# Optimization experiments

Hardware: AMD Instinct MI355X
Metric: run time of the kernel (lower is better)

Reference implementation:

```python
import jax, jax.numpy as jnp
import numpy as np

EPS = 1e-6

def act_quant(x):
    # per-token int8 absmax quantization with straight-through estimator
    scale = 127.0 / jnp.clip(jnp.max(jnp.abs(x), axis=-1, keepdims=True), 1e-5)
    q = jnp.clip(jnp.round(x * scale), -128.0, 127.0) / scale
    return x + jax.lax.stop_gradient(q - x)

def weight_quant(w):
    # ternary absmean quantization with straight-through estimator
    scale = 1.0 / jnp.clip(jnp.mean(jnp.abs(w)), 1e-5)
    q = jnp.clip(jnp.round(w * scale), -1.0, 1.0) / scale
    return w + jax.lax.stop_gradient(q - w)

def bit_linear(x, w):
    # x: [..., in], w: [out, in]
    return jnp.einsum('...i,oi->...o', act_quant(x), weight_quant(w))

def subln(x, g):
    # RMSNorm over last dim with learnable gain
    var = jnp.mean(jnp.square(x), axis=-1, keepdims=True)
    return x * jax.lax.rsqrt(var + EPS) * g

def setup_inputs() -> dict:
    key = jax.random.key(0)
    k1, k2, k3 = jax.random.split(key, 3)
    B, S, H, I = 8, 8192, 512, 2048
    x = jax.random.normal(k1, (B, S, H), dtype=jnp.float32)
    w_up = jax.random.normal(k2, (I, H), dtype=jnp.float32) * (H ** -0.5)
    w_down = jax.random.normal(k3, (H, I), dtype=jnp.float32) * (I ** -0.5)
    g = jnp.ones((I,), dtype=jnp.float32)
    return {'x': x, 'w_up': w_up, 'w_down': w_down, 'g': g}

def reference(x, w_up, w_down, g):
    h = bit_linear(x, w_up)            # [B,S,I]
    h = jnp.square(jax.nn.relu(h))     # relu^2 activation
    h = subln(h, g)                    # SubLN (RMSNorm)
    return bit_linear(h, w_down)       # [B,S,H]
```

## Files before the change

### kernel.cpp

```cpp
#include <hip/hip_runtime.h>
#include <stdint.h>


typedef int v4i __attribute__((ext_vector_type(4)));

#define AS1(p) ((const __attribute__((address_space(1))) void*)(p))
#define AS3(p) ((__attribute__((address_space(3))) void*)(p))

static constexpr size_t OFF_PART = 256;
static constexpr size_t OFF_SX   = 8192;
static constexpr size_t OFF_RSQ  = OFF_SX   + 262144;
static constexpr size_t OFF_S2   = OFF_RSQ  + 262144;
static constexpr size_t OFF_INV2 = OFF_S2   + 262144;
static constexpr size_t OFF_WUQ  = OFF_INV2 + 262144;
static constexpr size_t OFF_WDQ  = OFF_WUQ  + 1048576;
static constexpr size_t OFF_XQ   = OFF_WDQ  + 1048576;
static constexpr size_t OFF_HQ   = OFF_XQ   + 33554432;
static constexpr size_t OFF_SS   = OFF_HQ   + 134217728;
static constexpr size_t OFF_MM   = OFF_SS   + 8388608;

__global__ void wabs_partial(const float* __restrict__ w, double* __restrict__ part)
{
    int t = threadIdx.x, bid = blockIdx.x;
    const float4* w4 = (const float4*)w;
    int base = bid * 256 + t;
    double s = 0.0;
    #pragma unroll
    for (int j = 0; j < 4; ++j) {
        float4 v = w4[base + j * 65536];
        s += (double)fabsf(v.x) + (double)fabsf(v.y)
           + (double)fabsf(v.z) + (double)fabsf(v.w);
    }
    #pragma unroll
    for (int off = 32; off > 0; off >>= 1) s += __shfl_down(s, off);
    __shared__ double ps[4];
    int l = t & 63, wv = t >> 6;
    if (l == 0) ps[wv] = s;
    __syncthreads();
    if (t == 0) part[bid] = ((ps[0] + ps[1]) + ps[2]) + ps[3];
}

__global__ void finalize_sums(const double* __restrict__ part, double* __restrict__ sums)
{
    int t = threadIdx.x;
    double a = part[t];
    double b = part[256 + t];
    #pragma unroll
    for (int off = 32; off > 0; off >>= 1) {
        a += __shfl_down(a, off);
        b += __shfl_down(b, off);
    }
    __shared__ double pa[4], pb[4];
    int l = t & 63, wv = t >> 6;
    if (l == 0) { pa[wv] = a; pb[wv] = b; }
    __syncthreads();
    if (t == 0) {
        sums[0] = ((pa[0] + pa[1]) + pa[2]) + pa[3];
        sums[1] = ((pb[0] + pb[1]) + pb[2]) + pb[3];
    }
}

__global__ void wquant(const float* __restrict__ w, const double* __restrict__ sum,
                       signed char* __restrict__ wq)
{
    int i = blockIdx.x * blockDim.x + threadIdx.x;
    if (i >= 262144) return;
    float mean  = (float)(*sum) * (1.0f / 1048576.0f);
    float scale = 1.0f / fmaxf(mean, 1e-5f);
    float4 v = ((const float4*)w)[i];
    int q0 = (int)fminf(fmaxf(rintf(v.x * scale), -1.f), 1.f);
    int q1 = (int)fminf(fmaxf(rintf(v.y * scale), -1.f), 1.f);
    int q2 = (int)fminf(fmaxf(rintf(v.z * scale), -1.f), 1.f);
    int q3 = (int)fminf(fmaxf(rintf(v.w * scale), -1.f), 1.f);
    unsigned pk = (q0 & 255) | ((q1 & 255) << 8) | ((q2 & 255) << 16) | ((q3 & 255) << 24);
    ((unsigned*)wq)[i] = pk;
}

__global__ void xquant(const float* __restrict__ x, signed char* __restrict__ xq,
                       float* __restrict__ inv_sx)
{
    int row = blockIdx.x * 4 + (threadIdx.x >> 6);
    int l   = threadIdx.x & 63;
    const float* xr = x + (size_t)row * 512;
    float4 v0 = *(const float4*)(xr + l * 8);
    float4 v1 = *(const float4*)(xr + l * 8 + 4);
    float m = fmaxf(fmaxf(fmaxf(fabsf(v0.x), fabsf(v0.y)), fmaxf(fabsf(v0.z), fabsf(v0.w))),
                    fmaxf(fmaxf(fabsf(v1.x), fabsf(v1.y)), fmaxf(fabsf(v1.z), fabsf(v1.w))));
    #pragma unroll
    for (int off = 1; off < 64; off <<= 1) m = fmaxf(m, __shfl_xor(m, off));
    float mc = fmaxf(m, 1e-5f);
    float s  = 127.0f / mc;
    int q[8];
    q[0] = (int)fminf(fmaxf(rintf(v0.x * s), -128.f), 127.f);
    q[1] = (int)fminf(fmaxf(rintf(v0.y * s), -128.f), 127.f);
    q[2] = (int)fminf(fmaxf(rintf(v0.z * s), -128.f), 127.f);
    q[3] = (int)fminf(fmaxf(rintf(v0.w * s), -128.f), 127.f);
    q[4] = (int)fminf(fmaxf(rintf(v1.x * s), -128.f), 127.f);
    q[5] = (int)fminf(fmaxf(rintf(v1.y * s), -128.f), 127.f);
    q[6] = (int)fminf(fmaxf(rintf(v1.z * s), -128.f), 127.f);
    q[7] = (int)fminf(fmaxf(rintf(v1.w * s), -128.f), 127.f);
    uint2 pk;
    pk.x = (q[0] & 255) | ((q[1] & 255) << 8) | ((q[2] & 255) << 16) | ((q[3] & 255) << 24);
    pk.y = (q[4] & 255) | ((q[5] & 255) << 8) | ((q[6] & 255) << 16) | ((q[7] & 255) << 24);
    *(uint2*)(xq + (size_t)row * 512 + l * 8) = pk;
    if (l == 0) inv_sx[row] = mc * (1.0f / 127.0f);
}

__global__ void row_reduce(const float* __restrict__ ss_p, const float* __restrict__ mm_p,
                           float* __restrict__ rsq, float* __restrict__ s2,
                           float* __restrict__ inv2)
{
    int row = blockIdx.x * blockDim.x + threadIdx.x;
    float ss = 0.f, mm = 0.f;
    #pragma unroll
    for (int p = 0; p < 32; ++p) {
        ss += ss_p[(size_t)row * 32 + p];
        mm  = fmaxf(mm, mm_p[(size_t)row * 32 + p]);
    }
    float var  = ss * (1.0f / 2048.0f);
    float r    = 1.0f / sqrtf(var + 1e-6f);
    float maxy = fmaxf(r * mm, 1e-5f);
    rsq[row]  = r;
    s2[row]   = 127.0f / maxy;
    inv2[row] = maxy * (1.0f / 127.0f);
}


#define PHASE(MH, NH, STAGE_STMT, TAIL_STMT)                                   \
  {                                                                            \
    v4i af[8]; v4i bf[4];                                                      \
    _Pragma("unroll")                                                          \
    for (int mm = 0; mm < 4; ++mm) {                                           \
      _Pragma("unroll")                                                        \
      for (int ks = 0; ks < 2; ++ks) {                                         \
        int r  = wr * 128 + ((MH) * 4 + mm) * 16 + lr;                         \
        int eg = (ks * 4 + lg) ^ lx;                                           \
        af[mm * 2 + ks] = *(const v4i*)(Ab + r * 128 + eg * 16);               \
      }                                                                        \
    }                                                                          \
    _Pragma("unroll")                                                          \
    for (int nn = 0; nn < 2; ++nn) {                                           \
      _Pragma("unroll")                                                        \
      for (int ks = 0; ks < 2; ++ks) {                                         \
        int r  = wc * 64 + ((NH) * 2 + nn) * 16 + lr;                          \
        int eg = (ks * 4 + lg) ^ lx;                                           \
        bf[nn * 2 + ks] = *(const v4i*)(Bb + r * 128 + eg * 16);               \
      }                                                                        \
    }                                                                          \
    STAGE_STMT;                                                                \
    __builtin_amdgcn_s_barrier();                                              \
    asm volatile("s_waitcnt lgkmcnt(0)" ::: "memory");                         \
    __builtin_amdgcn_sched_barrier(0);                                         \
    __builtin_amdgcn_s_setprio(1);                                             \
    _Pragma("unroll")                                                          \
    for (int mm = 0; mm < 4; ++mm)                                             \
      _Pragma("unroll")                                                        \
      for (int nn = 0; nn < 2; ++nn)                                           \
        _Pragma("unroll")                                                      \
        for (int ks = 0; ks < 2; ++ks)                                         \
          acc[(MH) * 4 + mm][(NH) * 2 + nn] =                                  \
              __builtin_amdgcn_mfma_i32_16x16x64_i8(                           \
                  af[mm * 2 + ks], bf[nn * 2 + ks],                            \
                  acc[(MH) * 4 + mm][(NH) * 2 + nn], 0, 0, 0);                 \
    __builtin_amdgcn_s_setprio(0);                                             \
    TAIL_STMT;                                                                 \
    __builtin_amdgcn_s_barrier();                                              \
  }

#define KTILE(KT, P)                                                           \
  {                                                                            \
    const char* Ab = &lds[P][0][0];                                            \
    const char* Bb = &lds[P][1][0];                                            \
    const int kt_ = (KT);                                                      \
    PHASE(0, 0, { if (kt_ + 1 < NKT) stageA((P) ^ 1, 1, kt_ + 1); }, {})       \
    PHASE(0, 1, { if (kt_ + 1 < NKT) stageB((P) ^ 1, 1, kt_ + 1); }, {})       \
    PHASE(1, 0, { if (kt_ + 2 < NKT) stageA((P), 0, kt_ + 2); }, {})           \
    PHASE(1, 1, { if (kt_ + 2 < NKT) stageB((P), 0, kt_ + 2); },               \
          {                                                                    \
            if (kt_ < NKT - 1) {                                               \
              if (kt_ + 2 < NKT)                                               \
                asm volatile("s_waitcnt vmcnt(4)" ::: "memory");               \
              else                                                             \
                asm volatile("s_waitcnt vmcnt(0)" ::: "memory");               \
            }                                                                  \
          })                                                                   \
  }

template<int K, int N, int EPI>
__global__ __launch_bounds__(512, 2)
void gemm_i8(const signed char* __restrict__ A,
             const signed char* __restrict__ B,
             const float* __restrict__ rowscale,
             const double* __restrict__ wsum,
             const float* __restrict__ g,
             const float* __restrict__ rsq,
             const float* __restrict__ s2,
             float* __restrict__ st_ss,
             float* __restrict__ st_mm,
             signed char* __restrict__ hq,
             float* __restrict__ out)
{
    constexpr int NKT = K / 128;
    constexpr int NBN = N / 256;
    __shared__ __align__(16) char lds[2][2][32768];

    int nwg  = gridDim.x;
    int orig = blockIdx.x;
    int q8 = nwg >> 3, r8 = nwg & 7;
    int xcd = orig & 7, lin = orig >> 3;
    int swz = (xcd < r8 ? xcd * (q8 + 1) : r8 * (q8 + 1) + (xcd - r8) * q8) + lin;
    int mt = swz / NBN, nt = swz - mt * NBN;

    size_t mbase = (size_t)mt * 256;
    int    nbase = nt * 256;

    int t  = threadIdx.x;
    int l  = t & 63;
    int wid = t >> 6;
    int wr = wid >> 2, wc = wid & 3;
    int lr = l & 15, lg = l >> 4, lx = l & 7;

    const signed char* Ag = A + mbase * K;
    const signed char* Bg = B + (size_t)nbase * K;

    auto stageA = [&](int buf, int sel, int ktt) {
        char* d0 = &lds[buf][0][0];
        #pragma unroll
        for (int i = 0; i < 2; ++i) {
            int j = i * 512 + t;
            int rho = j >> 3, gg = j & 7;
            int r = rho + (rho & 64) + sel * 64;
            int kg = gg ^ (r & 7);
            __builtin_amdgcn_global_load_lds(AS1(Ag + (size_t)r * K + ktt * 128 + kg * 16),
                                             AS3(d0 + r * 128 + gg * 16), 16, 0, 0);
        }
    };
    auto stageB = [&](int buf, int sel, int ktt) {
        char* d0 = &lds[buf][1][0];
        #pragma unroll
        for (int i = 0; i < 2; ++i) {
            int j = i * 512 + t;
            int rho = j >> 3, gg = j & 7;
            int r = ((rho & ~31) << 1) + (rho & 31) + sel * 32;
            int kg = gg ^ (r & 7);
            __builtin_amdgcn_global_load_lds(AS1(Bg + (size_t)r * K + ktt * 128 + kg * 16),
                                             AS3(d0 + r * 128 + gg * 16), 16, 0, 0);
        }
    };

    v4i acc[8][4] = {};

    stageA(0, 0, 0); stageB(0, 0, 0); stageA(0, 1, 0); stageB(0, 1, 0);
    if (NKT > 1) {
        stageA(1, 0, 1); stageB(1, 0, 1);
        asm volatile("s_waitcnt vmcnt(4)" ::: "memory");
    } else {
        asm volatile("s_waitcnt vmcnt(0)" ::: "memory");
    }
    __builtin_amdgcn_s_barrier();

    #pragma unroll 1
    for (int kt2 = 0; kt2 < NKT / 2; ++kt2) {
        int kt = kt2 * 2;
        KTILE(kt, 0)
        KTILE(kt + 1, 1)
    }

    float wmean = fmaxf((float)wsum[0] * (1.0f / 1048576.0f), 1e-5f);
    size_t rowb = mbase + (size_t)wr * 128;
    int    colb = nbase + wc * 64;

    if constexpr (EPI == 2) {
        #pragma unroll
        for (int m = 0; m < 8; ++m)
            #pragma unroll
            for (int reg = 0; reg < 4; ++reg) {
                size_t grow = rowb + m * 16 + lg * 4 + reg;
                float f = rowscale[grow] * wmean;
                #pragma unroll
                for (int n = 0; n < 4; ++n)
                    out[grow * N + colb + n * 16 + lr] = (float)acc[m][n][reg] * f;
            }
    } else {
        float gv[4];
        #pragma unroll
        for (int n = 0; n < 4; ++n) gv[n] = g[colb + n * 16 + lr];

        if constexpr (EPI == 0) {
            #pragma unroll
            for (int m = 0; m < 8; ++m)
                #pragma unroll
                for (int reg = 0; reg < 4; ++reg) {
                    size_t grow = rowb + m * 16 + lg * 4 + reg;
                    float f = rowscale[grow] * wmean;
                    float ss = 0.f, mx = 0.f;
                    #pragma unroll
                    for (int n = 0; n < 4; ++n) {
                        float z = (float)acc[m][n][reg] * f;
                        float a = fmaxf(z, 0.f);
                        float h = a * a;
                        ss += h * h;
                        mx  = fmaxf(mx, fabsf(h * gv[n]));
                    }
                    #pragma unroll
                    for (int off = 1; off < 16; off <<= 1) {
                        ss += __shfl_xor(ss, off);
                        mx  = fmaxf(mx, __shfl_xor(mx, off));
                    }
                    if (lr == 0) {
                        st_ss[grow * 32 + nt * 4 + wc] = ss;
                        st_mm[grow * 32 + nt * 4 + wc] = mx;
                    }
                }
        } else {
            #pragma unroll
            for (int m = 0; m < 8; ++m)
                #pragma unroll
                for (int reg = 0; reg < 4; ++reg) {
                    size_t grow = rowb + m * 16 + lg * 4 + reg;
                    float f  = rowscale[grow] * wmean;
                    float rq = rsq[grow];
                    float sc = s2[grow];
                    #pragma unroll
                    for (int n = 0; n < 4; ++n) {
                        float z = (float)acc[m][n][reg] * f;
                        float a = fmaxf(z, 0.f);
                        float h = a * a;
                        float y = (h * rq) * gv[n];
                        int qv = (int)fminf(fmaxf(rintf(y * sc), -128.f), 127.f);
                        hq[grow * 2048 + colb + n * 16 + lr] = (signed char)qv;
                    }
                }
        }
    }
}

extern "C" void kernel_launch(void* const* d_in, const int* in_sizes, int n_in,
                              void* d_out, int out_size, void* d_ws, size_t ws_size,
                              hipStream_t stream)
{
    const float* x  = (const float*)d_in[0];
    const float* wu = (const float*)d_in[1];
    const float* wd = (const float*)d_in[2];
    const float* g  = (const float*)d_in[3];
    float* out = (float*)d_out;
    char*  ws  = (char*)d_ws;

    double* sums     = (double*)ws;
    double* part     = (double*)(ws + OFF_PART);
    float*  inv_sx   = (float*)(ws + OFF_SX);
    float*  rsq      = (float*)(ws + OFF_RSQ);
    float*  s2       = (float*)(ws + OFF_S2);
    float*  inv2     = (float*)(ws + OFF_INV2);
    signed char* wuq = (signed char*)(ws + OFF_WUQ);
    signed char* wdq = (signed char*)(ws + OFF_WDQ);
    signed char* xq  = (signed char*)(ws + OFF_XQ);
    signed char* hq  = (signed char*)(ws + OFF_HQ);
    float*  st_ss    = (float*)(ws + OFF_SS);
    float*  st_mm    = (float*)(ws + OFF_MM);

    wabs_partial<<<256, 256, 0, stream>>>(wu, part);
    wabs_partial<<<256, 256, 0, stream>>>(wd, part + 256);
    finalize_sums<<<1, 256, 0, stream>>>(part, sums);
    wquant<<<1024, 256, 0, stream>>>(wu, sums + 0, wuq);
    wquant<<<1024, 256, 0, stream>>>(wd, sums + 1, wdq);
    xquant<<<16384, 256, 0, stream>>>(x, xq, inv_sx);

    gemm_i8<512, 2048, 0><<<2048, 512, 0, stream>>>(xq, wuq, inv_sx, sums + 0, g,
                                                    nullptr, nullptr, st_ss, st_mm,
                                                    nullptr, nullptr);
    row_reduce<<<256, 256, 0, stream>>>(st_ss, st_mm, rsq, s2, inv2);
    gemm_i8<512, 2048, 1><<<2048, 512, 0, stream>>>(xq, wuq, inv_sx, sums + 0, g,
                                                    rsq, s2, nullptr, nullptr,
                                                    hq, nullptr);
    gemm_i8<2048, 512, 2><<<512, 512, 0, stream>>>(hq, wdq, inv2, sums + 1,
                                                   nullptr, nullptr, nullptr,
                                                   nullptr, nullptr, nullptr, out);
}
```

Measured before the change: 597.2 us.

## Switch int8 GEMM to 32x32x32 MFMA with K=64 tiles and simpler pipeline

Replaces the 16x16x64 int8 MFMA tiling with 32x32x32 MFMA instructions, halving the K-tile to 64 bytes and shrinking LDS from 128KB to 64KB. The hand-tuned four-phase pipeline with split A/B staging, setprio and fine-grained vmcnt waits is replaced by a simple double buffer with __syncthreads between stages. Epilogue index mapping and the row reduction shuffle width change to match the 32x32 accumulator layout. The aim is fewer LDS fragment reads per MFMA and lower LDS footprint, at the cost of losing the finer overlap of loads and compute.

```diff
diff --git a/kernel.cpp b/kernel.cpp
--- a/kernel.cpp
+++ b/kernel.cpp
@@ -2,7 +2,8 @@
 #include <stdint.h>
 
 
-typedef int v4i __attribute__((ext_vector_type(4)));
+typedef int v4i  __attribute__((ext_vector_type(4)));
+typedef int v16i __attribute__((ext_vector_type(16)));
 
 #define AS1(p) ((const __attribute__((address_space(1))) void*)(p))
 #define AS3(p) ((__attribute__((address_space(3))) void*)(p))
@@ -126,64 +127,32 @@
 }
 
 
-#define PHASE(MH, NH, STAGE_STMT, TAIL_STMT)                                   \
-  {                                                                            \
-    v4i af[8]; v4i bf[4];                                                      \
-    _Pragma("unroll")                                                          \
-    for (int mm = 0; mm < 4; ++mm) {                                           \
-      _Pragma("unroll")                                                        \
-      for (int ks = 0; ks < 2; ++ks) {                                         \
-        int r  = wr * 128 + ((MH) * 4 + mm) * 16 + lr;                         \
-        int eg = (ks * 4 + lg) ^ lx;                                           \
-        af[mm * 2 + ks] = *(const v4i*)(Ab + r * 128 + eg * 16);               \
-      }                                                                        \
-    }                                                                          \
-    _Pragma("unroll")                                                          \
-    for (int nn = 0; nn < 2; ++nn) {                                           \
-      _Pragma("unroll")                                                        \
-      for (int ks = 0; ks < 2; ++ks) {                                         \
-        int r  = wc * 64 + ((NH) * 2 + nn) * 16 + lr;                          \
-        int eg = (ks * 4 + lg) ^ lx;                                           \
-        bf[nn * 2 + ks] = *(const v4i*)(Bb + r * 128 + eg * 16);               \
-      }                                                                        \
-    }                                                                          \
-    STAGE_STMT;                                                                \
-    __builtin_amdgcn_s_barrier();                                              \
-    asm volatile("s_waitcnt lgkmcnt(0)" ::: "memory");                         \
-    __builtin_amdgcn_sched_barrier(0);                                         \
-    __builtin_amdgcn_s_setprio(1);                                             \
-    _Pragma("unroll")                                                          \
-    for (int mm = 0; mm < 4; ++mm)                                             \
-      _Pragma("unroll")                                                        \
-      for (int nn = 0; nn < 2; ++nn)                                           \
-        _Pragma("unroll")                                                      \
-        for (int ks = 0; ks < 2; ++ks)                                         \
-          acc[(MH) * 4 + mm][(NH) * 2 + nn] =                                  \
-              __builtin_amdgcn_mfma_i32_16x16x64_i8(                           \
-                  af[mm * 2 + ks], bf[nn * 2 + ks],                            \
-                  acc[(MH) * 4 + mm][(NH) * 2 + nn], 0, 0, 0);                 \
-    __builtin_amdgcn_s_setprio(0);                                             \
-    TAIL_STMT;                                                                 \
-    __builtin_amdgcn_s_barrier();                                              \
-  }
-
-#define KTILE(KT, P)                                                           \
+#define COMPUTE(P)                                                             \
   {                                                                            \
     const char* Ab = &lds[P][0][0];                                            \
     const char* Bb = &lds[P][1][0];                                            \
-    const int kt_ = (KT);                                                      \
-    PHASE(0, 0, { if (kt_ + 1 < NKT) stageA((P) ^ 1, 1, kt_ + 1); }, {})       \
-    PHASE(0, 1, { if (kt_ + 1 < NKT) stageB((P) ^ 1, 1, kt_ + 1); }, {})       \
-    PHASE(1, 0, { if (kt_ + 2 < NKT) stageA((P), 0, kt_ + 2); }, {})           \
-    PHASE(1, 1, { if (kt_ + 2 < NKT) stageB((P), 0, kt_ + 2); },               \
-          {                                                                    \
-            if (kt_ < NKT - 1) {                                               \
-              if (kt_ + 2 < NKT)                                               \
-                asm volatile("s_waitcnt vmcnt(4)" ::: "memory");               \
-              else                                                             \
-                asm volatile("s_waitcnt vmcnt(0)" ::: "memory");               \
-            }                                                                  \
-          })                                                                   \
+    _Pragma("unroll")                                                          \
+    for (int ks = 0; ks < 2; ++ks) {                                           \
+      v4i af[4]; v4i bf[2];                                                    \
+      _Pragma("unroll")                                                        \
+      for (int m = 0; m < 4; ++m) {                                            \
+        int r  = wr * 128 + m * 32 + lr;                                       \
+        int eg = (ks * 2 + lh) ^ (r & 3);                                      \
+        af[m] = *(const v4i*)(Ab + r * 64 + eg * 16);                          \
+      }                                                                        \
+      _Pragma("unroll")                                                        \
+      for (int n = 0; n < 2; ++n) {                                            \
+        int r  = wc * 64 + n * 32 + lr;                                        \
+        int eg = (ks * 2 + lh) ^ (r & 3);                                      \
+        bf[n] = *(const v4i*)(Bb + r * 64 + eg * 16);                          \
+      }                                                                        \
+      _Pragma("unroll")                                                        \
+      for (int m = 0; m < 4; ++m)                                              \
+        _Pragma("unroll")                                                      \
+        for (int n = 0; n < 2; ++n)                                            \
+          acc[m][n] = __builtin_amdgcn_mfma_i32_32x32x32_i8(                   \
+              af[m], bf[n], acc[m][n], 0, 0, 0);                               \
+    }                                                                          \
   }
 
 template<int K, int N, int EPI>
@@ -200,9 +169,9 @@
              signed char* __restrict__ hq,
              float* __restrict__ out)
 {
-    constexpr int NKT = K / 128;
+    constexpr int NKT = K / 64;
     constexpr int NBN = N / 256;
-    __shared__ __align__(16) char lds[2][2][32768];
+    __shared__ __align__(16) char lds[2][2][16384];
 
     int nwg  = gridDim.x;
     int orig = blockIdx.x;
@@ -218,52 +187,44 @@
     int l  = t & 63;
     int wid = t >> 6;
     int wr = wid >> 2, wc = wid & 3;
-    int lr = l & 15, lg = l >> 4, lx = l & 7;
+    int lr = l & 31, lh = l >> 5;
 
     const signed char* Ag = A + mbase * K;
     const signed char* Bg = B + (size_t)nbase * K;
 
-    auto stageA = [&](int buf, int sel, int ktt) {
-        char* d0 = &lds[buf][0][0];
+    auto stage = [&](int buf, int kt) {
         #pragma unroll
         for (int i = 0; i < 2; ++i) {
             int j = i * 512 + t;
-            int rho = j >> 3, gg = j & 7;
-            int r = rho + (rho & 64) + sel * 64;
-            int kg = gg ^ (r & 7);
-            __builtin_amdgcn_global_load_lds(AS1(Ag + (size_t)r * K + ktt * 128 + kg * 16),
-                                             AS3(d0 + r * 128 + gg * 16), 16, 0, 0);
+            int r = j >> 2, gg = j & 3;
+            int kg = gg ^ (r & 3);
+            __builtin_amdgcn_global_load_lds(AS1(Ag + (size_t)r * K + kt * 64 + kg * 16),
+                                             AS3(&lds[buf][0][0] + j * 16), 16, 0, 0);
         }
-    };
-    auto stageB = [&](int buf, int sel, int ktt) {
-        char* d0 = &lds[buf][1][0];
         #pragma unroll
         for (int i = 0; i < 2; ++i) {
             int j = i * 512 + t;
-            int rho = j >> 3, gg = j & 7;
-            int r = ((rho & ~31) << 1) + (rho & 31) + sel * 32;
-            int kg = gg ^ (r & 7);
-            __builtin_amdgcn_global_load_lds(AS1(Bg + (size_t)r * K + ktt * 128 + kg * 16),
-                                             AS3(d0 + r * 128 + gg * 16), 16, 0, 0);
+            int r = j >> 2, gg = j & 3;
+            int kg = gg ^ (r & 3);
+            __builtin_amdgcn_global_load_lds(AS1(Bg + (size_t)r * K + kt * 64 + kg * 16),
+                                             AS3(&lds[buf][1][0] + j * 16), 16, 0, 0);
         }
     };
 
-    v4i acc[8][4] = {};
-
-    stageA(0, 0, 0); stageB(0, 0, 0); stageA(0, 1, 0); stageB(0, 1, 0);
-    if (NKT > 1) {
-        stageA(1, 0, 1); stageB(1, 0, 1);
-        asm volatile("s_waitcnt vmcnt(4)" ::: "memory");
-    } else {
-        asm volatile("s_waitcnt vmcnt(0)" ::: "memory");
-    }
-    __builtin_amdgcn_s_barrier();
+    v16i acc[4][2] = {};
+
+    stage(0, 0);
+    __syncthreads();
 
     #pragma unroll 1
     for (int kt2 = 0; kt2 < NKT / 2; ++kt2) {
         int kt = kt2 * 2;
-        KTILE(kt, 0)
-        KTILE(kt + 1, 1)
+        stage(1, kt + 1);
+        COMPUTE(0)
+        __syncthreads();
+        if (kt + 2 < NKT) stage(0, kt + 2);
+        COMPUTE(1)
+        __syncthreads();
     }
 
     float wmean = fmaxf((float)wsum[0] * (1.0f / 1048576.0f), 1e-5f);
@@ -272,30 +233,30 @@
 
     if constexpr (EPI == 2) {
         #pragma unroll
-        for (int m = 0; m < 8; ++m)
+        for (int m = 0; m < 4; ++m)
             #pragma unroll
-            for (int reg = 0; reg < 4; ++reg) {
-                size_t grow = rowb + m * 16 + lg * 4 + reg;
+            for (int reg = 0; reg < 16; ++reg) {
+                size_t grow = rowb + m * 32 + (reg & 3) + 8 * (reg >> 2) + 4 * lh;
                 float f = rowscale[grow] * wmean;
                 #pragma unroll
-                for (int n = 0; n < 4; ++n)
-                    out[grow * N + colb + n * 16 + lr] = (float)acc[m][n][reg] * f;
+                for (int n = 0; n < 2; ++n)
+                    out[grow * N + colb + n * 32 + lr] = (float)acc[m][n][reg] * f;
             }
     } else {
-        float gv[4];
+        float gv[2];
         #pragma unroll
-        for (int n = 0; n < 4; ++n) gv[n] = g[colb + n * 16 + lr];
+        for (int n = 0; n < 2; ++n) gv[n] = g[colb + n * 32 + lr];
 
         if constexpr (EPI == 0) {
             #pragma unroll
-            for (int m = 0; m < 8; ++m)
+            for (int m = 0; m < 4; ++m)
                 #pragma unroll
-                for (int reg = 0; reg < 4; ++reg) {
-                    size_t grow = rowb + m * 16 + lg * 4 + reg;
+                for (int reg = 0; reg < 16; ++reg) {
+                    size_t grow = rowb + m * 32 + (reg & 3) + 8 * (reg >> 2) + 4 * lh;
                     float f = rowscale[grow] * wmean;
                     float ss = 0.f, mx = 0.f;
                     #pragma unroll
-                    for (int n = 0; n < 4; ++n) {
+                    for (int n = 0; n < 2; ++n) {
                         float z = (float)acc[m][n][reg] * f;
                         float a = fmaxf(z, 0.f);
                         float h = a * a;
@@ -303,7 +264,7 @@
                         mx  = fmaxf(mx, fabsf(h * gv[n]));
                     }
                     #pragma unroll
-                    for (int off = 1; off < 16; off <<= 1) {
+                    for (int off = 1; off < 32; off <<= 1) {
                         ss += __shfl_xor(ss, off);
                         mx  = fmaxf(mx, __shfl_xor(mx, off));
                     }
@@ -314,21 +275,21 @@
                 }
         } else {
             #pragma unroll
-            for (int m = 0; m < 8; ++m)
+            for (int m = 0; m < 4; ++m)
                 #pragma unroll
-                for (int reg = 0; reg < 4; ++reg) {
-                    size_t grow = rowb + m * 16 + lg * 4 + reg;
+                for (int reg = 0; reg < 16; ++reg) {
+                    size_t grow = rowb + m * 32 + (reg & 3) + 8 * (reg >> 2) + 4 * lh;
                     float f  = rowscale[grow] * wmean;
                     float rq = rsq[grow];
                     float sc = s2[grow];
                     #pragma unroll
-                    for (int n = 0; n < 4; ++n) {
+                    for (int n = 0; n < 2; ++n) {
                         float z = (float)acc[m][n][reg] * f;
                         float a = fmaxf(z, 0.f);
                         float h = a * a;
                         float y = (h * rq) * gv[n];
                         int qv = (int)fminf(fmaxf(rintf(y * sc), -128.f), 127.f);
-                        hq[grow * 2048 + colb + n * 16 + lr] = (signed char)qv;
+                        hq[grow * 2048 + colb + n * 32 + lr] = (signed char)qv;
                     }
                 }
         }
```

Measured after the change: 693.7 us. 1.16x slower.
